# Kernel optimization log

Hardware: AMD Instinct MI355X
Metric: run time of the kernel (lower is better)

Reference implementation:

```python
import jax, jax.numpy as jnp
import numpy as np

N, E = 50000, 640000
D_IN, D_HID, D_OUT, HEADS = 128, 128, 128, 2


def _lin_init(k, fan_in, fan_out):
    return jax.random.normal(k, (fan_in, fan_out), jnp.float32) / np.sqrt(fan_in)


def setup_inputs() -> dict:
    key = jax.random.key(0)
    ks = jax.random.split(key, 20)
    inp = {
        "x": jax.random.normal(ks[0], (N, D_IN), jnp.float32),
        "edge_index": jax.random.randint(ks[1], (2, E), 0, N, dtype=jnp.int32),
    }
    # layer 1: in -> hid (heads*per_head = 2 * 64 = 128)
    inp["Wq1"] = _lin_init(ks[2], D_IN, D_HID); inp["bq1"] = jnp.zeros((D_HID,), jnp.float32)
    inp["Wk1"] = _lin_init(ks[3], D_IN, D_HID); inp["bk1"] = jnp.zeros((D_HID,), jnp.float32)
    inp["Wv1"] = _lin_init(ks[4], D_IN, D_HID); inp["bv1"] = jnp.zeros((D_HID,), jnp.float32)
    inp["Ws1"] = _lin_init(ks[5], D_IN, D_HID); inp["bs1"] = jnp.zeros((D_HID,), jnp.float32)
    # layer 2: hid -> out
    inp["Wq2"] = _lin_init(ks[6], D_HID, D_OUT); inp["bq2"] = jnp.zeros((D_OUT,), jnp.float32)
    inp["Wk2"] = _lin_init(ks[7], D_HID, D_OUT); inp["bk2"] = jnp.zeros((D_OUT,), jnp.float32)
    inp["Wv2"] = _lin_init(ks[8], D_HID, D_OUT); inp["bv2"] = jnp.zeros((D_OUT,), jnp.float32)
    inp["Ws2"] = _lin_init(ks[9], D_HID, D_OUT); inp["bs2"] = jnp.zeros((D_OUT,), jnp.float32)
    return inp


def _transformer_conv(x, src, dst, Wq, bq, Wk, bk, Wv, bv, Ws, bs, heads):
    """PyG TransformerConv (concat=True, root_weight=True, eval mode)."""
    n = x.shape[0]
    C = Wq.shape[1] // heads  # per-head channels
    q = (x @ Wq + bq).reshape(n, heads, C)
    k = (x @ Wk + bk).reshape(n, heads, C)
    v = (x @ Wv + bv).reshape(n, heads, C)
    qi = q[dst]              # [E, H, C] gather at destination
    kj = k[src]              # [E, H, C] gather at source
    vj = v[src]              # [E, H, C]
    alpha = jnp.sum(qi * kj, axis=-1) / np.sqrt(C)   # [E, H]
    # segment softmax over incoming edges of each destination node
    amax = jax.ops.segment_max(alpha, dst, num_segments=n)   # [N, H]
    ex = jnp.exp(alpha - amax[dst])                            # [E, H]
    denom = jax.ops.segment_sum(ex, dst, num_segments=n)      # [N, H]
    a = ex / denom[dst]                                        # [E, H]
    msg = vj * a[..., None]                                    # [E, H, C]
    out = jax.ops.segment_sum(msg, dst, num_segments=n).reshape(n, heads * C)
    return out + x @ Ws + bs  # root (skip) connection


def reference(x, edge_index, Wq1, bq1, Wk1, bk1, Wv1, bv1, Ws1, bs1,
              Wq2, bq2, Wk2, bk2, Wv2, bv2, Ws2, bs2):
    src, dst = edge_index[0], edge_index[1]
    h = _transformer_conv(x, src, dst, Wq1, bq1, Wk1, bk1, Wv1, bv1, Ws1, bs1, HEADS)
    h = jax.nn.relu(h)
    return _transformer_conv(h, src, dst, Wq2, bq2, Wk2, bk2, Wv2, bv2, Ws2, bs2, HEADS)
```

## Files before the change

kernel.cpp:

```cpp
#include <hip/hip_runtime.h>
#include <math.h>

#define D 128

typedef float  f32x4  __attribute__((ext_vector_type(4)));
typedef short  bf16x8 __attribute__((ext_vector_type(8)));

__device__ inline unsigned short bf16r(float f) {
    unsigned u = __float_as_uint(f);
    u = (u + 0x7fff + ((u >> 16) & 1)) >> 16;
    return (unsigned short)u;
}
__device__ inline unsigned bf16pair(float a, float b) {
    return (unsigned)bf16r(a) | ((unsigned)bf16r(b) << 16);
}
__device__ inline float bf16lo(unsigned w) { return __uint_as_float(w << 16); }
__device__ inline float bf16hi(unsigned w) { return __uint_as_float(w & 0xffff0000u); }

__device__ inline void unpack8(uint4 w, float* f) {
    f[0] = bf16lo(w.x); f[1] = bf16hi(w.x);
    f[2] = bf16lo(w.y); f[3] = bf16hi(w.y);
    f[4] = bf16lo(w.z); f[5] = bf16hi(w.z);
    f[6] = bf16lo(w.w); f[7] = bf16hi(w.w);
}

__global__ __launch_bounds__(256)
void prep(const float* __restrict__ X, unsigned* __restrict__ Xb, int npairs,
          const float* __restrict__ W0, const float* __restrict__ W1,
          const float* __restrict__ W2, const float* __restrict__ W3,
          const float* __restrict__ W4, const float* __restrict__ W5,
          const float* __restrict__ W6, const float* __restrict__ W7,
          unsigned short* __restrict__ Wt,
          int* __restrict__ cnt, int* __restrict__ cursor,
          int* __restrict__ bh, int* __restrict__ bcur, int n)
{
    const int nxb = (npairs + 255) >> 8;
    const int nz  = (n + 255) >> 8;
    const int b = blockIdx.x;
    if (b < nxb) {
        int i = b * 256 + threadIdx.x;
        if (i < npairs) {
            float2 v = *(const float2*)&X[2 * i];
            Xb[i] = bf16pair(v.x, v.y);
        }
    } else if (b < nxb + nz) {
        int i = (b - nxb) * 256 + threadIdx.x;
        if (i < n) { cnt[i] = 0; cursor[i] = 0; }
    } else if (b < nxb + nz + 8) {
        int wi = b - nxb - nz;
        const float* Ws[8] = {W0, W1, W2, W3, W4, W5, W6, W7};
        const float* W = Ws[wi];
        unsigned short* o = Wt + wi * 16384;
        for (int i = threadIdx.x; i < 16384; i += 256) {
            int k = i >> 7, c = i & 127;
            o[c * 128 + k] = bf16r(W[i]);
        }
    } else {
        if (threadIdx.x < 64) { bh[threadIdx.x] = 0; bcur[threadIdx.x] = 0; }
    }
}

__global__ __launch_bounds__(256)
void gemm_mfma(const unsigned short* __restrict__ Xb, int n,
               const unsigned short* __restrict__ Wtall,
               const float* __restrict__ bq, const float* __restrict__ bk,
               const float* __restrict__ bv, const float* __restrict__ bs,
               unsigned short* __restrict__ Qp, unsigned short* __restrict__ Kp,
               unsigned short* __restrict__ Vp, unsigned short* __restrict__ Sp)
{
    const int w = blockIdx.x;
    const int rowBase = blockIdx.y * 128;
    const unsigned short* W = Wtall + w * 16384;
    const float* bias = (w == 0) ? bq : (w == 1) ? bk : (w == 2) ? bv : bs;
    unsigned short* plane = (w == 0) ? Qp : (w == 1) ? Kp : (w == 2) ? Vp : Sp;

    __shared__ unsigned short Asm[128 * 136];

    const int tid  = threadIdx.x;
    const int wave = tid >> 6;
    const int lane = tid & 63;
    const int wr   = wave >> 1;
    const int wc   = wave & 1;
    const int q16  = lane >> 4;
    const int r16  = lane & 15;

    #pragma unroll
    for (int i = 0; i < 8; ++i) {
        int g = tid + 256 * i;
        int m = g >> 4, c = g & 15;
        int row = rowBase + m; if (row >= n) row = n - 1;
        uint4 da = *(const uint4*)(Xb + (size_t)row * 128 + c * 8);
        *(uint4*)&Asm[m * 136 + c * 8] = da;
    }

    const unsigned short* Wbase = W + (size_t)(wc * 64 + r16) * 128 + q16 * 8;
    bf16x8 bcur[4], bnxt[4];
    #pragma unroll
    for (int nj = 0; nj < 4; ++nj)
        bcur[nj] = *(const bf16x8*)(Wbase + nj * 16 * 128);

    __syncthreads();

    f32x4 acc[4][4];
    #pragma unroll
    for (int mi = 0; mi < 4; ++mi)
        #pragma unroll
        for (int nj = 0; nj < 4; ++nj) acc[mi][nj] = (f32x4)(0.f);

    #pragma unroll
    for (int kc = 0; kc < 4; ++kc) {
        if (kc < 3) {
            #pragma unroll
            for (int nj = 0; nj < 4; ++nj)
                bnxt[nj] = *(const bf16x8*)(Wbase + nj * 16 * 128 + (kc + 1) * 32);
        }
        bf16x8 a[4];
        #pragma unroll
        for (int mi = 0; mi < 4; ++mi)
            a[mi] = *(const bf16x8*)&Asm[(wr * 64 + mi * 16 + r16) * 136 + kc * 32 + q16 * 8];
        #pragma unroll
        for (int mi = 0; mi < 4; ++mi)
            #pragma unroll
            for (int nj = 0; nj < 4; ++nj)
                acc[mi][nj] = __builtin_amdgcn_mfma_f32_16x16x32_bf16(a[mi], bcur[nj], acc[mi][nj], 0, 0, 0);
        #pragma unroll
        for (int nj = 0; nj < 4; ++nj) bcur[nj] = bnxt[nj];
    }

    __syncthreads();
    #pragma unroll
    for (int nj = 0; nj < 4; ++nj) {
        const int col = wc * 64 + nj * 16 + r16;
        const float bias_c = bias[col];
        #pragma unroll
        for (int mi = 0; mi < 4; ++mi) {
            const int rbase = wr * 64 + mi * 16 + q16 * 4;
            #pragma unroll
            for (int r = 0; r < 4; ++r)
                Asm[(rbase + r) * 132 + col] = bf16r(acc[mi][nj][r] + bias_c);
        }
    }
    __syncthreads();
    #pragma unroll
    for (int i = 0; i < 8; ++i) {
        int g = tid + 256 * i;
        int m = g >> 4, c = g & 15;
        int row = rowBase + m;
        if (row < n) {
            uint4 d2 = *(const uint4*)&Asm[m * 132 + c * 8];
            *(uint4*)(plane + (size_t)row * 128 + c * 8) = d2;
        }
    }
}

__global__ void degree_hist(const int* __restrict__ dst, int e, int* __restrict__ cnt)
{
    int i = blockIdx.x * blockDim.x + threadIdx.x;
    if (i < e) atomicAdd(&cnt[dst[i]], 1);
}

__global__ __launch_bounds__(256)
void scan_hist(const int* __restrict__ cnt, int n, int* __restrict__ bsum, int* __restrict__ bh)
{
    __shared__ int sm[256];
    __shared__ int lh[64];
    if (threadIdx.x < 64) lh[threadIdx.x] = 0;
    int i = blockIdx.x * 256 + threadIdx.x;
    int v = (i < n) ? cnt[i] : 0;
    sm[threadIdx.x] = v;
    __syncthreads();
    if (i < n) atomicAdd(&lh[min(v, 63)], 1);
    #pragma unroll
    for (int off = 128; off > 0; off >>= 1) {
        if (threadIdx.x < off) sm[threadIdx.x] += sm[threadIdx.x + off];
        __syncthreads();
    }
    if (threadIdx.x == 0) bsum[blockIdx.x] = sm[0];
    if (threadIdx.x < 64 && lh[threadIdx.x] > 0)
        atomicAdd(&bh[threadIdx.x], lh[threadIdx.x]);
}

__global__ __launch_bounds__(256)
void scan2(int* __restrict__ bsum, int nb, const int* __restrict__ bh, int* __restrict__ boff)
{
    __shared__ int sm[256];
    int v = (threadIdx.x < nb) ? bsum[threadIdx.x] : 0;
    sm[threadIdx.x] = v;
    __syncthreads();
    int acc = v;
    for (int off = 1; off < 256; off <<= 1) {
        int t = (threadIdx.x >= off) ? sm[threadIdx.x - off] : 0;
        __syncthreads();
        acc += t;
        sm[threadIdx.x] = acc;
        __syncthreads();
    }
    if (threadIdx.x < nb) bsum[threadIdx.x] = acc - v;
    if (threadIdx.x == 0) {
        int run = 0;
        for (int b = 63; b >= 0; --b) { boff[b] = run; run += bh[b]; }
    }
}

__global__ __launch_bounds__(256)
void scan3_scatter(const int* __restrict__ cnt, const int* __restrict__ bsum,
                   int* __restrict__ row_ptr, int n, int e,
                   const int* __restrict__ boff, int* __restrict__ bcur,
                   int* __restrict__ perm)
{
    __shared__ int sm[256];
    __shared__ int lh[64];
    __shared__ int lbase[64];
    if (threadIdx.x < 64) lh[threadIdx.x] = 0;
    __syncthreads();
    int i = blockIdx.x * 256 + threadIdx.x;
    int v = (i < n) ? cnt[i] : 0;
    sm[threadIdx.x] = v;
    int b = 0, local = 0;
    if (i < n) {
        b = min(v, 63);
        local = atomicAdd(&lh[b], 1);
    }
    __syncthreads();
    int acc = v;
    for (int off = 1; off < 256; off <<= 1) {
        int t = (threadIdx.x >= off) ? sm[threadIdx.x - off] : 0;
        __syncthreads();
        acc += t;
        sm[threadIdx.x] = acc;
        __syncthreads();
    }
    if (i < n) row_ptr[i] = bsum[blockIdx.x] + acc - v;
    if (blockIdx.x == 0 && threadIdx.x == 0) row_ptr[n] = e;
    if (threadIdx.x < 64 && lh[threadIdx.x] > 0)
        lbase[threadIdx.x] = atomicAdd(&bcur[threadIdx.x], lh[threadIdx.x]);
    __syncthreads();
    if (i < n) perm[boff[b] + lbase[b] + local] = i;
}

__global__ void edge_scatter(const int* __restrict__ src, const int* __restrict__ dst, int e,
                             const int* __restrict__ row_ptr, int* __restrict__ cursor,
                             int* __restrict__ csr_src)
{
    int i = blockIdx.x * blockDim.x + threadIdx.x;
    if (i < e) {
        int d = dst[i];
        int pos = atomicAdd(&cursor[d], 1);
        csr_src[row_ptr[d] + pos] = src[i];
    }
}

__global__ __launch_bounds__(256)
void attn(const uint4* __restrict__ Qp, const uint4* __restrict__ Kp,
          const uint4* __restrict__ Vp, const uint4* __restrict__ Sp,
          const int* __restrict__ row_ptr, const int* __restrict__ csr_src,
          const int* __restrict__ perm,
          float* __restrict__ outf, uint4* __restrict__ outb,
          int n, int do_relu)
{
    const int wid  = (blockIdx.x * 256 + threadIdx.x) >> 6;
    const int lane = threadIdx.x & 63;
    const int nq   = lane >> 4;
    const int l16  = lane & 15;
    const int nidx = wid * 4 + nq;
    const int node = (nidx < n) ? perm[nidx] : -1;

    float q[8];
    int beg = 0, end = 0;
    if (node >= 0) {
        uint4 qw = Qp[(size_t)node * 16 + l16];
        unpack8(qw, q);
        beg = row_ptr[node];
        end = row_ptr[node + 1];
    }

    float m = -INFINITY, l = 0.f;
    float acc[8] = {0.f, 0.f, 0.f, 0.f, 0.f, 0.f, 0.f, 0.f};

    int i = beg;
    uint4 kw = make_uint4(0, 0, 0, 0), vw = make_uint4(0, 0, 0, 0);
    if (i < end) {
        int s = csr_src[i];
        kw = Kp[(size_t)s * 16 + l16];
        vw = Vp[(size_t)s * 16 + l16];
    }
    while (i < end) {
        uint4 kc = kw, vc = vw;
        if (i + 1 < end) {
            int s2 = csr_src[i + 1];
            kw = Kp[(size_t)s2 * 16 + l16];
            vw = Vp[(size_t)s2 * 16 + l16];
        }
        float kf[8], vf[8];
        unpack8(kc, kf);
        unpack8(vc, vf);
        float part = q[0]*kf[0] + q[1]*kf[1] + q[2]*kf[2] + q[3]*kf[3]
                   + q[4]*kf[4] + q[5]*kf[5] + q[6]*kf[6] + q[7]*kf[7];
        part += __shfl_xor(part, 4, 64);
        part += __shfl_xor(part, 2, 64);
        part += __shfl_xor(part, 1, 64);
        float alpha = part * 0.125f;
        float mn = fmaxf(m, alpha);
        float corr = __expf(m - mn);
        float p = __expf(alpha - mn);
        l = l * corr + p;
        #pragma unroll
        for (int c2 = 0; c2 < 8; ++c2) acc[c2] = acc[c2] * corr + p * vf[c2];
        m = mn;
        ++i;
    }

    if (node >= 0) {
        float inv = (l > 0.f) ? (1.f / l) : 0.f;
        float sv[8];
        unpack8(Sp[(size_t)node * 16 + l16], sv);
        float r[8];
        #pragma unroll
        for (int c2 = 0; c2 < 8; ++c2) r[c2] = acc[c2] * inv + sv[c2];
        if (do_relu) {
            #pragma unroll
            for (int c2 = 0; c2 < 8; ++c2) r[c2] = fmaxf(r[c2], 0.f);
        }
        if (outb) {
            uint4 o;
            o.x = bf16pair(r[0], r[1]); o.y = bf16pair(r[2], r[3]);
            o.z = bf16pair(r[4], r[5]); o.w = bf16pair(r[6], r[7]);
            outb[(size_t)node * 16 + l16] = o;
        } else {
            *(float4*)&outf[(size_t)node * 128 + l16 * 8]     = make_float4(r[0], r[1], r[2], r[3]);
            *(float4*)&outf[(size_t)node * 128 + l16 * 8 + 4] = make_float4(r[4], r[5], r[6], r[7]);
        }
    }
}

extern "C" void kernel_launch(void* const* d_in, const int* in_sizes, int n_in,
                              void* d_out, int out_size, void* d_ws, size_t ws_size,
                              hipStream_t stream)
{
    const float* x    = (const float*)d_in[0];
    const int*   edge = (const int*)d_in[1];
    const int n = in_sizes[0] / D;
    const int e = in_sizes[1] / 2;
    const int* srcv = edge;
    const int* dstv = edge + e;

    const float* Wq1 = (const float*)d_in[2];  const float* bq1 = (const float*)d_in[3];
    const float* Wk1 = (const float*)d_in[4];  const float* bk1 = (const float*)d_in[5];
    const float* Wv1 = (const float*)d_in[6];  const float* bv1 = (const float*)d_in[7];
    const float* Ws1 = (const float*)d_in[8];  const float* bs1 = (const float*)d_in[9];
    const float* Wq2 = (const float*)d_in[10]; const float* bq2 = (const float*)d_in[11];
    const float* Wk2 = (const float*)d_in[12]; const float* bk2 = (const float*)d_in[13];
    const float* Wv2 = (const float*)d_in[14]; const float* bv2 = (const float*)d_in[15];
    const float* Ws2 = (const float*)d_in[16]; const float* bs2 = (const float*)d_in[17];

    char* wsb = (char*)d_ws;
    size_t off = 0;
    auto alloc = [&](size_t bytes) -> void* {
        void* p = wsb + off;
        off += (bytes + 255) & ~(size_t)255;
        return p;
    };
    unsigned short* Qp = (unsigned short*)alloc((size_t)n * D * sizeof(unsigned short));
    unsigned short* Kp = (unsigned short*)alloc((size_t)n * D * sizeof(unsigned short));
    unsigned short* Vp = (unsigned short*)alloc((size_t)n * D * sizeof(unsigned short));
    unsigned short* Sp = (unsigned short*)alloc((size_t)n * D * sizeof(unsigned short));
    unsigned short* Xb = (unsigned short*)alloc((size_t)n * D * sizeof(unsigned short));
    unsigned short* Hu = (unsigned short*)alloc((size_t)n * D * sizeof(unsigned short));
    unsigned short* Wt = (unsigned short*)alloc(8 * 16384 * sizeof(unsigned short));
    int* cnt     = (int*)alloc((size_t)n * sizeof(int));
    int* cursor  = (int*)alloc((size_t)n * sizeof(int));
    int* row_ptr = (int*)alloc((size_t)(n + 1) * sizeof(int));
    int* bsum    = (int*)alloc(1024 * sizeof(int));
    int* perm    = (int*)alloc((size_t)n * sizeof(int));
    int* bh      = (int*)alloc(64 * sizeof(int));
    int* bcur    = (int*)alloc(64 * sizeof(int));
    int* boff    = (int*)alloc(64 * sizeof(int));
    int* csr_src = (int*)alloc((size_t)e * sizeof(int));
    (void)ws_size; (void)n_in; (void)out_size;

    const int nb  = (n + 255) / 256;
    const int npairs = n * 64;
    const int nprep  = (npairs + 255) / 256 + nb + 8 + 1;

    prep<<<nprep, 256, 0, stream>>>(x, (unsigned*)Xb, npairs,
        Wq1, Wk1, Wv1, Ws1, Wq2, Wk2, Wv2, Ws2, Wt, cnt, cursor, bh, bcur, n);

    degree_hist<<<(e + 255) / 256, 256, 0, stream>>>(dstv, e, cnt);
    scan_hist<<<nb, 256, 0, stream>>>(cnt, n, bsum, bh);
    scan2<<<1, 256, 0, stream>>>(bsum, nb, bh, boff);
    scan3_scatter<<<nb, 256, 0, stream>>>(cnt, bsum, row_ptr, n, e, boff, bcur, perm);
    edge_scatter<<<(e + 255) / 256, 256, 0, stream>>>(srcv, dstv, e, row_ptr, cursor, csr_src);

    const dim3 ggrid(4, (n + 127) / 128);
    const int ablocks = ((n + 3) / 4 + 3) / 4;

    gemm_mfma<<<ggrid, 256, 0, stream>>>(Xb, n, Wt, bq1, bk1, bv1, bs1, Qp, Kp, Vp, Sp);
    attn<<<ablocks, 256, 0, stream>>>((const uint4*)Qp, (const uint4*)Kp, (const uint4*)Vp,
                                      (const uint4*)Sp, row_ptr, csr_src, perm,
                                      nullptr, (uint4*)Hu, n, 1);

    gemm_mfma<<<ggrid, 256, 0, stream>>>(Hu, n, Wt + 4 * 16384, bq2, bk2, bv2, bs2, Qp, Kp, Vp, Sp);
    attn<<<ablocks, 256, 0, stream>>>((const uint4*)Qp, (const uint4*)Kp, (const uint4*)Vp,
                                      (const uint4*)Sp, row_ptr, csr_src, perm,
                                      (float*)d_out, nullptr, n, 0);
}
```

Before: 357.1 us.

## Batch four edges per attention step and reuse histogram atomics for CSR ranks

The attention loop now loads the K/V rows of four neighbors at once and applies a single online-softmax rescale per group of four, with a scalar tail loop for the remainder. This raises memory-level parallelism in the gather-bound loop, replacing the previous one-ahead prefetch, at the cost of more registers. The degree histogram also records each edge's atomic return value as its rank within the destination. Edge scatter then writes directly without a second atomic pass or a cursor array, adding one E-sized int array.

```diff
diff --git a/kernel.cpp b/kernel.cpp
--- a/kernel.cpp
+++ b/kernel.cpp
@@ -31,8 +31,7 @@
           const float* __restrict__ W4, const float* __restrict__ W5,
           const float* __restrict__ W6, const float* __restrict__ W7,
           unsigned short* __restrict__ Wt,
-          int* __restrict__ cnt, int* __restrict__ cursor,
-          int* __restrict__ bh, int* __restrict__ bcur, int n)
+          int* __restrict__ cnt, int* __restrict__ bh, int* __restrict__ bcur, int n)
 {
     const int nxb = (npairs + 255) >> 8;
     const int nz  = (n + 255) >> 8;
@@ -45,7 +44,7 @@
         }
     } else if (b < nxb + nz) {
         int i = (b - nxb) * 256 + threadIdx.x;
-        if (i < n) { cnt[i] = 0; cursor[i] = 0; }
+        if (i < n) cnt[i] = 0;
     } else if (b < nxb + nz + 8) {
         int wi = b - nxb - nz;
         const float* Ws[8] = {W0, W1, W2, W3, W4, W5, W6, W7};
@@ -153,10 +152,11 @@
     }
 }
 
-__global__ void degree_hist(const int* __restrict__ dst, int e, int* __restrict__ cnt)
+__global__ void degree_hist(const int* __restrict__ dst, int e,
+                            int* __restrict__ cnt, int* __restrict__ rank)
 {
     int i = blockIdx.x * blockDim.x + threadIdx.x;
-    if (i < e) atomicAdd(&cnt[dst[i]], 1);
+    if (i < e) rank[i] = atomicAdd(&cnt[dst[i]], 1);
 }
 
 __global__ __launch_bounds__(256)
@@ -239,14 +239,13 @@
 }
 
 __global__ void edge_scatter(const int* __restrict__ src, const int* __restrict__ dst, int e,
-                             const int* __restrict__ row_ptr, int* __restrict__ cursor,
+                             const int* __restrict__ row_ptr, const int* __restrict__ rank,
                              int* __restrict__ csr_src)
 {
     int i = blockIdx.x * blockDim.x + threadIdx.x;
     if (i < e) {
         int d = dst[i];
-        int pos = atomicAdd(&cursor[d], 1);
-        csr_src[row_ptr[d] + pos] = src[i];
+        csr_src[row_ptr[d] + rank[i]] = src[i];
     }
 }
 
@@ -278,24 +277,61 @@
     float acc[8] = {0.f, 0.f, 0.f, 0.f, 0.f, 0.f, 0.f, 0.f};
 
     int i = beg;
-    uint4 kw = make_uint4(0, 0, 0, 0), vw = make_uint4(0, 0, 0, 0);
-    if (i < end) {
+    while (i + 4 <= end) {
+        int s0 = csr_src[i], s1 = csr_src[i+1], s2 = csr_src[i+2], s3 = csr_src[i+3];
+        uint4 kw0 = Kp[(size_t)s0 * 16 + l16];
+        uint4 kw1 = Kp[(size_t)s1 * 16 + l16];
+        uint4 kw2 = Kp[(size_t)s2 * 16 + l16];
+        uint4 kw3 = Kp[(size_t)s3 * 16 + l16];
+        uint4 vw0 = Vp[(size_t)s0 * 16 + l16];
+        uint4 vw1 = Vp[(size_t)s1 * 16 + l16];
+        uint4 vw2 = Vp[(size_t)s2 * 16 + l16];
+        uint4 vw3 = Vp[(size_t)s3 * 16 + l16];
+
+        float kf[8];
+        unpack8(kw0, kf);
+        float d0 = q[0]*kf[0]+q[1]*kf[1]+q[2]*kf[2]+q[3]*kf[3]+q[4]*kf[4]+q[5]*kf[5]+q[6]*kf[6]+q[7]*kf[7];
+        unpack8(kw1, kf);
+        float d1 = q[0]*kf[0]+q[1]*kf[1]+q[2]*kf[2]+q[3]*kf[3]+q[4]*kf[4]+q[5]*kf[5]+q[6]*kf[6]+q[7]*kf[7];
+        unpack8(kw2, kf);
+        float d2 = q[0]*kf[0]+q[1]*kf[1]+q[2]*kf[2]+q[3]*kf[3]+q[4]*kf[4]+q[5]*kf[5]+q[6]*kf[6]+q[7]*kf[7];
+        unpack8(kw3, kf);
+        float d3 = q[0]*kf[0]+q[1]*kf[1]+q[2]*kf[2]+q[3]*kf[3]+q[4]*kf[4]+q[5]*kf[5]+q[6]*kf[6]+q[7]*kf[7];
+
+        d0 += __shfl_xor(d0, 4, 64); d1 += __shfl_xor(d1, 4, 64);
+        d2 += __shfl_xor(d2, 4, 64); d3 += __shfl_xor(d3, 4, 64);
+        d0 += __shfl_xor(d0, 2, 64); d1 += __shfl_xor(d1, 2, 64);
+        d2 += __shfl_xor(d2, 2, 64); d3 += __shfl_xor(d3, 2, 64);
+        d0 += __shfl_xor(d0, 1, 64); d1 += __shfl_xor(d1, 1, 64);
+        d2 += __shfl_xor(d2, 1, 64); d3 += __shfl_xor(d3, 1, 64);
+
+        float a0 = d0 * 0.125f, a1 = d1 * 0.125f, a2 = d2 * 0.125f, a3 = d3 * 0.125f;
+        float m4 = fmaxf(fmaxf(a0, a1), fmaxf(a2, a3));
+        float mn = fmaxf(m, m4);
+        float corr = __expf(m - mn);
+        float p0 = __expf(a0 - mn), p1 = __expf(a1 - mn);
+        float p2 = __expf(a2 - mn), p3 = __expf(a3 - mn);
+        l = l * corr + (p0 + p1 + p2 + p3);
+
+        float v0f[8], v1f[8], v2f[8], v3f[8];
+        unpack8(vw0, v0f); unpack8(vw1, v1f); unpack8(vw2, v2f); unpack8(vw3, v3f);
+        #pragma unroll
+        for (int c2 = 0; c2 < 8; ++c2) {
+            float t = acc[c2] * corr;
+            t += p0 * v0f[c2]; t += p1 * v1f[c2];
+            t += p2 * v2f[c2]; t += p3 * v3f[c2];
+            acc[c2] = t;
+        }
+        m = mn;
+        i += 4;
+    }
+    while (i < end) {
         int s = csr_src[i];
-        kw = Kp[(size_t)s * 16 + l16];
-        vw = Vp[(size_t)s * 16 + l16];
-    }
-    while (i < end) {
-        uint4 kc = kw, vc = vw;
-        if (i + 1 < end) {
-            int s2 = csr_src[i + 1];
-            kw = Kp[(size_t)s2 * 16 + l16];
-            vw = Vp[(size_t)s2 * 16 + l16];
-        }
+        uint4 kw = Kp[(size_t)s * 16 + l16];
+        uint4 vw = Vp[(size_t)s * 16 + l16];
         float kf[8], vf[8];
-        unpack8(kc, kf);
-        unpack8(vc, vf);
-        float part = q[0]*kf[0] + q[1]*kf[1] + q[2]*kf[2] + q[3]*kf[3]
-                   + q[4]*kf[4] + q[5]*kf[5] + q[6]*kf[6] + q[7]*kf[7];
+        unpack8(kw, kf); unpack8(vw, vf);
+        float part = q[0]*kf[0]+q[1]*kf[1]+q[2]*kf[2]+q[3]*kf[3]+q[4]*kf[4]+q[5]*kf[5]+q[6]*kf[6]+q[7]*kf[7];
         part += __shfl_xor(part, 4, 64);
         part += __shfl_xor(part, 2, 64);
         part += __shfl_xor(part, 1, 64);
@@ -368,13 +404,13 @@
     unsigned short* Hu = (unsigned short*)alloc((size_t)n * D * sizeof(unsigned short));
     unsigned short* Wt = (unsigned short*)alloc(8 * 16384 * sizeof(unsigned short));
     int* cnt     = (int*)alloc((size_t)n * sizeof(int));
-    int* cursor  = (int*)alloc((size_t)n * sizeof(int));
     int* row_ptr = (int*)alloc((size_t)(n + 1) * sizeof(int));
     int* bsum    = (int*)alloc(1024 * sizeof(int));
     int* perm    = (int*)alloc((size_t)n * sizeof(int));
     int* bh      = (int*)alloc(64 * sizeof(int));
     int* bcur    = (int*)alloc(64 * sizeof(int));
     int* boff    = (int*)alloc(64 * sizeof(int));
+    int* rank    = (int*)alloc((size_t)e * sizeof(int));
     int* csr_src = (int*)alloc((size_t)e * sizeof(int));
     (void)ws_size; (void)n_in; (void)out_size;
 
@@ -383,13 +419,13 @@
     const int nprep  = (npairs + 255) / 256 + nb + 8 + 1;
 
     prep<<<nprep, 256, 0, stream>>>(x, (unsigned*)Xb, npairs,
-        Wq1, Wk1, Wv1, Ws1, Wq2, Wk2, Wv2, Ws2, Wt, cnt, cursor, bh, bcur, n);
-
-    degree_hist<<<(e + 255) / 256, 256, 0, stream>>>(dstv, e, cnt);
+        Wq1, Wk1, Wv1, Ws1, Wq2, Wk2, Wv2, Ws2, Wt, cnt, bh, bcur, n);
+
+    degree_hist<<<(e + 255) / 256, 256, 0, stream>>>(dstv, e, cnt, rank);
     scan_hist<<<nb, 256, 0, stream>>>(cnt, n, bsum, bh);
     scan2<<<1, 256, 0, stream>>>(bsum, nb, bh, boff);
     scan3_scatter<<<nb, 256, 0, stream>>>(cnt, bsum, row_ptr, n, e, boff, bcur, perm);
-    edge_scatter<<<(e + 255) / 256, 256, 0, stream>>>(srcv, dstv, e, row_ptr, cursor, csr_src);
+    edge_scatter<<<(e + 255) / 256, 256, 0, stream>>>(srcv, dstv, e, row_ptr, rank, csr_src);
 
     const dim3 ggrid(4, (n + 127) / 128);
     const int ablocks = ((n + 3) / 4 + 3) / 4;
```

Result: faster. 338.0 us (-5.4%).
